# Kernel optimization log

Measured on AMD Instinct MI355X. Metric: run time of the kernel, lower is better.

Reference implementation:

```python
import jax, jax.numpy as jnp
import numpy as np

D_MODEL = 1024
NUM_HEADS = 16
HEAD_DIM = D_MODEL // NUM_HEADS


def setup_inputs() -> dict:
    key = jax.random.key(0)
    k_x, k_wqkv, k_bqkv, k_wo, k_bo = jax.random.split(key, 5)
    B, T = 2, 2048
    x = jax.random.normal(k_x, (B, T, D_MODEL), dtype=jnp.float32)
    # flax Dense default: lecun_normal kernel, zero bias; we use scaled normal for kernels
    w_qkv = jax.random.normal(k_wqkv, (D_MODEL, 3 * D_MODEL), dtype=jnp.float32) / np.sqrt(D_MODEL)
    b_qkv = jnp.zeros((3 * D_MODEL,), dtype=jnp.float32)
    w_out = jax.random.normal(k_wo, (D_MODEL, D_MODEL), dtype=jnp.float32) / np.sqrt(D_MODEL)
    b_out = jnp.zeros((D_MODEL,), dtype=jnp.float32)
    return {"x": x, "w_qkv": w_qkv, "b_qkv": b_qkv, "w_out": w_out, "b_out": b_out}


def reference(x, w_qkv, b_qkv, w_out, b_out):
    B, T, C = x.shape
    H, D = NUM_HEADS, HEAD_DIM
    qkv = x @ w_qkv + b_qkv                      # [B,T,3C]
    q, k, v = jnp.split(qkv, 3, axis=-1)         # each [B,T,C]

    def split_heads(t):
        return t.reshape(B, T, H, D).transpose(0, 2, 1, 3)  # [B,H,T,D]

    q, k, v = split_heads(q), split_heads(k), split_heads(v)
    attn = jnp.einsum('bhqd,bhkd->bhqk', q, k) / jnp.sqrt(jnp.float32(D))
    attn = jax.nn.softmax(attn, axis=-1)
    out = jnp.einsum('bhqk,bhkd->bhqd', attn, v)  # [B,H,T,D]
    out = out.transpose(0, 2, 1, 3).reshape(B, T, H * D)
    return out @ w_out + b_out
```

## Files before the change

### kernel.cpp

```cpp
#include <hip/hip_runtime.h>
#include <math.h>

#define D_MODEL 1024
#define NHEAD   16
#define HDIM    64
#define BATCH   2
#define SEQ     2048
#define M_TOTAL (BATCH*SEQ)

typedef _Float16 f16;
typedef _Float16 f16x4 __attribute__((ext_vector_type(4)));
typedef _Float16 f16x8 __attribute__((ext_vector_type(8)));
typedef float    f32x4 __attribute__((ext_vector_type(4)));

#if __has_builtin(__builtin_amdgcn_exp2f)
#define EXP2F(x) __builtin_amdgcn_exp2f(x)
#else
#define EXP2F(x) exp2f(x)
#endif

#define QSCALE 0.18033688011112042f

__device__ __forceinline__ void gl2lds16(const f16* g, f16* l) {
    __builtin_amdgcn_global_load_lds(
        (const __attribute__((address_space(1))) void*)g,
        (__attribute__((address_space(3))) void*)l,
        16, 0, 0);
}

__global__ __launch_bounds__(256) void convert_x_kernel(
    const float* __restrict__ x, f16* __restrict__ xh, int n4)
{
    int i = blockIdx.x * 256 + threadIdx.x;
    if (i >= n4) return;
    float4 v = ((const float4*)x)[i];
    f16x4 hv = {(f16)v.x, (f16)v.y, (f16)v.z, (f16)v.w};
    *(f16x4*)&xh[(size_t)i * 4] = hv;
}

__global__ __launch_bounds__(256) void convert_wt_kernel(
    const float* __restrict__ W, f16* __restrict__ Wth, int K, int N)
{
    __shared__ float tile[64][65];
    const int n0 = blockIdx.x * 64, k0 = blockIdx.y * 64;
    const int tx = threadIdx.x & 15, ty = threadIdx.x >> 4;
    #pragma unroll
    for (int i = 0; i < 4; ++i) {
        float4 v = *(const float4*)&W[(size_t)(k0 + ty + 16*i) * N + n0 + tx*4];
        tile[ty + 16*i][tx*4 + 0] = v.x;
        tile[ty + 16*i][tx*4 + 1] = v.y;
        tile[ty + 16*i][tx*4 + 2] = v.z;
        tile[ty + 16*i][tx*4 + 3] = v.w;
    }
    __syncthreads();
    #pragma unroll
    for (int i = 0; i < 4; ++i) {
        int n = ty + 16*i;
        f16x4 hv = {(f16)tile[tx*4 + 0][n], (f16)tile[tx*4 + 1][n],
                    (f16)tile[tx*4 + 2][n], (f16)tile[tx*4 + 3][n]};
        *(f16x4*)&Wth[(size_t)(n0 + n) * K + k0 + tx*4] = hv;
    }
}

__global__ __launch_bounds__(256) void gemm_qkv_mfma(
    const f16* __restrict__ Ahg, const f16* __restrict__ Bhg,
    const float* __restrict__ bias,
    f16* __restrict__ Qf, f16* __restrict__ Kf, f16* __restrict__ Vt)
{
    const int K = 1024;
    const int flat = blockIdx.x;
    const int xcd  = flat & 7;
    const int idx  = flat >> 3;
    const int m_blk = (xcd >> 1) * 8  + (idx & 7);
    const int n_blk = (xcd & 1) * 12 + (idx >> 3);
    const int n0 = n_blk * 128;
    const int m0 = m_blk * 128;
    const int tid  = threadIdx.x;
    const int lane = tid & 63;
    const int wave = tid >> 6;
    const int quad = lane >> 4;
    const int txl  = lane & 15;
    const int wm = (wave >> 1) * 64;
    const int wn = (wave & 1) * 64;

    __shared__ __align__(16) f16 sAh[128*64];
    __shared__ __align__(16) f16 sBh[128*64];

    f32x4 acc[4][4];
    #pragma unroll
    for (int i = 0; i < 4; ++i)
        #pragma unroll
        for (int j = 0; j < 4; ++j) { f32x4 z = {0.f,0.f,0.f,0.f}; acc[i][j] = z; }

    for (int kt = 0; kt < K; kt += 64) {
        __syncthreads();
        #pragma unroll
        for (int it = 0; it < 4; ++it) {
            int f = it*256 + tid;
            int r = f >> 3;
            int gc = (f & 7) ^ (r & 7);
            gl2lds16(&Ahg[(size_t)(m0 + r) * K + kt + gc*8], &sAh[f*8]);
            gl2lds16(&Bhg[(size_t)(n0 + r) * K + kt + gc*8], &sBh[f*8]);
        }
        __syncthreads();

        #pragma unroll
        for (int ks = 0; ks < 2; ++ks) {
            f16x8 ah[4], bh[4];
            #pragma unroll
            for (int i = 0; i < 4; ++i) {
                int r = wm + 16*i + txl;
                ah[i] = *(const f16x8*)&sAh[(r*8 + ((ks*4 + quad) ^ (r & 7))) * 8];
            }
            #pragma unroll
            for (int j = 0; j < 4; ++j) {
                int r = wn + 16*j + txl;
                bh[j] = *(const f16x8*)&sBh[(r*8 + ((ks*4 + quad) ^ (r & 7))) * 8];
            }
            #pragma unroll
            for (int j = 0; j < 4; ++j)
                #pragma unroll
                for (int i = 0; i < 4; ++i)
                    acc[i][j] = __builtin_amdgcn_mfma_f32_16x16x32_f16(ah[i], bh[j], acc[i][j], 0,0,0);
        }
    }

    #pragma unroll
    for (int j = 0; j < 4; ++j) {
        int n = n0 + wn + 16*j + txl;
        float bv = bias[n];
        int which = n >> 10;
        int h = (n >> 6) & 15;
        int d = n & 63;
        #pragma unroll
        for (int i = 0; i < 4; ++i) {
            int m0i = m0 + wm + 16*i + quad*4;
            int bb  = m0i >> 11;
            int t0  = m0i & (SEQ - 1);
            if (which == 2) {
                f16x4 pw = {(f16)(acc[i][j][0] + bv), (f16)(acc[i][j][1] + bv),
                            (f16)(acc[i][j][2] + bv), (f16)(acc[i][j][3] + bv)};
                *(f16x4*)&Vt[((size_t)(bb*NHEAD + h) * HDIM + d) * SEQ + t0] = pw;
            } else {
                #pragma unroll
                for (int rr = 0; rr < 4; ++rr) {
                    float v = acc[i][j][rr] + bv;
                    if (which == 0)
                        Qf[((size_t)(bb*NHEAD + h) * SEQ + t0 + rr) * HDIM + d] = (f16)(v * QSCALE);
                    else
                        Kf[((size_t)(bb*NHEAD + h) * SEQ + t0 + rr) * HDIM + d] = (f16)v;
                }
            }
        }
    }
}

__global__ __launch_bounds__(256, 4) void attn_mfma(
    const f16* __restrict__ Qf, const f16* __restrict__ Kf,
    const f16* __restrict__ Vt, f16* __restrict__ Oat)
{
    const int flat = blockIdx.x;
    const int xcd  = flat & 7;
    const int idx  = flat >> 3;
    const int bh = xcd*4 + (idx >> 5);
    const int qt = idx & 31;
    const int b  = bh >> 4;
    const int h  = bh & 15;
    const int tid  = threadIdx.x;
    const int lane = tid & 63;
    const int wave = tid >> 6;
    const int quad = lane >> 4;
    const int txl  = lane & 15;
    const int qh = wave >> 1;
    const int kh = wave & 1;

    __shared__ __align__(16) char smem[40960];
    f16* sQ  = (f16*)smem;
    f16* sKb = (f16*)(smem + 8*1024);
    f16* sVb = (f16*)(smem + 24*1024);
    float* sL      = (float*)smem;
    float* scratch = (float*)(smem + 8*1024);

    const f16* Qg = Qf + (size_t)bh * SEQ * HDIM + (size_t)qt * 64 * HDIM;
    const f16* Kg = Kf + (size_t)bh * SEQ * HDIM;
    const f16* Vg = Vt + (size_t)bh * HDIM * SEQ;

    #pragma unroll
    for (int it = 0; it < 2; ++it) {
        int f = it*256 + tid;
        int r = f >> 3;
        int gc = (f & 7) ^ (r & 7);
        gl2lds16(&Qg[(size_t)r * HDIM + gc*8], &sQ[f*8]);
        gl2lds16(&Kg[(size_t)r * HDIM + gc*8], &sKb[f*8]);
        gl2lds16(&Vg[(size_t)r * SEQ + gc*8], &sVb[f*8]);
    }
    __syncthreads();

    f16x8 bq[2][2];
    #pragma unroll
    for (int i = 0; i < 2; ++i) {
        int row = qh*32 + i*16 + txl;
        #pragma unroll
        for (int dc = 0; dc < 2; ++dc) {
            int cp = (dc*4 + quad) ^ (row & 7);
            bq[i][dc] = *(const f16x8*)&sQ[(row*8 + cp) * 8];
        }
    }
    __syncthreads();

    f32x4 oacc[2][4];
    f32x4 lmf[2];
    const f16x4 vones = {(f16)1.f, (f16)1.f, (f16)1.f, (f16)1.f};
    #pragma unroll
    for (int i = 0; i < 2; ++i) {
        f32x4 z = {0.f,0.f,0.f,0.f};
        lmf[i] = z;
        #pragma unroll
        for (int jn = 0; jn < 4; ++jn) oacc[i][jn] = z;
    }

    const int NT = SEQ / 64;
    #pragma unroll 2
    for (int t = 0; t < NT; ++t) {
        const f16* sKc = sKb + (t & 1) * 4096;
        const f16* sVc = sVb + (t & 1) * 4096;
        if (t + 1 < NT) {
            f16* sKn = sKb + ((t + 1) & 1) * 4096;
            f16* sVn = sVb + ((t + 1) & 1) * 4096;
            int kt2 = (t + 1) * 64;
            #pragma unroll
            for (int it = 0; it < 2; ++it) {
                int f = it*256 + tid;
                int r = f >> 3;
                int gc = (f & 7) ^ (r & 7);
                gl2lds16(&Kg[(size_t)(kt2 + r) * HDIM + gc*8], &sKn[f*8]);
                gl2lds16(&Vg[(size_t)r * SEQ + kt2 + gc*8], &sVn[f*8]);
            }
        }

        #pragma unroll
        for (int kg = 0; kg < 2; ++kg) {
            int krow = kh*32 + kg*16 + txl;
            f16x8 aK0 = *(const f16x8*)&sKc[(krow*8 + ((quad    ) ^ (krow & 7))) * 8];
            f16x8 aK1 = *(const f16x8*)&sKc[(krow*8 + ((quad + 4) ^ (krow & 7))) * 8];
            f16x4 bV[4];
            #pragma unroll
            for (int jn = 0; jn < 4; ++jn) {
                int d = jn*16 + txl;
                int slot = (kh*4 + kg*2 + (quad >> 1)) ^ (d & 7);
                bV[jn] = *(const f16x4*)&sVc[d*64 + slot*8 + (quad & 1)*4];
            }
            #pragma unroll
            for (int i = 0; i < 2; ++i) {
                f32x4 s = {0.f,0.f,0.f,0.f};
                s = __builtin_amdgcn_mfma_f32_16x16x32_f16(aK0, bq[i][0], s, 0,0,0);
                s = __builtin_amdgcn_mfma_f32_16x16x32_f16(aK1, bq[i][1], s, 0,0,0);
                float p0 = EXP2F(s[0]), p1 = EXP2F(s[1]);
                float p2 = EXP2F(s[2]), p3 = EXP2F(s[3]);
                f16x4 pa = {(f16)p0, (f16)p1, (f16)p2, (f16)p3};
                lmf[i] = __builtin_amdgcn_mfma_f32_16x16x16f16(pa, vones, lmf[i], 0,0,0);
                #pragma unroll
                for (int jn = 0; jn < 4; ++jn)
                    oacc[i][jn] = __builtin_amdgcn_mfma_f32_16x16x16f16(pa, bV[jn], oacc[i][jn], 0,0,0);
            }
        }
        __syncthreads();
    }

    if (txl == 0) {
        *(f32x4*)&sL[wave*32 +  0 + quad*4] = lmf[0];
        *(f32x4*)&sL[wave*32 + 16 + quad*4] = lmf[1];
    }
    __syncthreads();

    #pragma unroll
    for (int i = 0; i < 2; ++i) {
        #pragma unroll
        for (int jn = 0; jn < 4; ++jn) {
            int d = jn*16 + txl;
            *(f32x4*)&scratch[wave*1024 + d*16 + quad*4] = oacc[i][jn];
        }
        __syncthreads();
        const int d = tid & 63;
        const int g = tid >> 6;
        #pragma unroll
        for (int e = 0; e < 8; ++e) {
            int slot = g*8 + e;
            int hh = slot >> 4;
            int ql = slot & 15;
            float o = scratch[(2*hh)*1024 + d*16 + ql] + scratch[(2*hh+1)*1024 + d*16 + ql];
            float l = sL[(2*hh)*32 + i*16 + ql] + sL[(2*hh+1)*32 + i*16 + ql];
            int q = qt*64 + hh*32 + i*16 + ql;
            Oat[(size_t)(b*SEQ + q) * D_MODEL + h*HDIM + d] = (f16)(o / l);
        }
        __syncthreads();
    }
}

__global__ __launch_bounds__(256) void gemm_out_mfma(
    const f16* __restrict__ Ag, const f16* __restrict__ Bhg,
    const float* __restrict__ bias, float* __restrict__ Cg)
{
    const int K = 1024, N = 1024;
    const int flat = blockIdx.x;
    const int xcd  = flat & 7;
    const int idx  = flat >> 3;
    const int m0 = (xcd*8 + (idx & 7)) * 64;
    const int n0 = (idx >> 3) * 128;
    const int tid  = threadIdx.x;
    const int lane = tid & 63;
    const int wave = tid >> 6;
    const int quad = lane >> 4;
    const int txl  = lane & 15;
    const int wm = (wave >> 1) * 32;
    const int wn = (wave & 1) * 64;

    __shared__ __align__(16) f16 sA[64*64];
    __shared__ __align__(16) f16 sB[128*64];

    f32x4 acc[2][4];
    #pragma unroll
    for (int i = 0; i < 2; ++i)
        #pragma unroll
        for (int j = 0; j < 4; ++j) { f32x4 z = {0.f,0.f,0.f,0.f}; acc[i][j] = z; }

    for (int kt = 0; kt < K; kt += 64) {
        __syncthreads();
        #pragma unroll
        for (int it = 0; it < 2; ++it) {
            int f = it*256 + tid;
            int r = f >> 3;
            int gc = (f & 7) ^ (r & 7);
            gl2lds16(&Ag[(size_t)(m0 + r) * K + kt + gc*8], &sA[f*8]);
        }
        #pragma unroll
        for (int it = 0; it < 4; ++it) {
            int f = it*256 + tid;
            int r = f >> 3;
            int gc = (f & 7) ^ (r & 7);
            gl2lds16(&Bhg[(size_t)(n0 + r) * K + kt + gc*8], &sB[f*8]);
        }
        __syncthreads();

        #pragma unroll
        for (int ks = 0; ks < 2; ++ks) {
            f16x8 a[2], bb[4];
            #pragma unroll
            for (int i = 0; i < 2; ++i) {
                int r = wm + 16*i + txl;
                a[i] = *(const f16x8*)&sA[(r*8 + ((ks*4 + quad) ^ (r & 7))) * 8];
            }
            #pragma unroll
            for (int j = 0; j < 4; ++j) {
                int r = wn + 16*j + txl;
                bb[j] = *(const f16x8*)&sB[(r*8 + ((ks*4 + quad) ^ (r & 7))) * 8];
            }
            #pragma unroll
            for (int j = 0; j < 4; ++j)
                #pragma unroll
                for (int i = 0; i < 2; ++i)
                    acc[i][j] = __builtin_amdgcn_mfma_f32_16x16x32_f16(a[i], bb[j], acc[i][j], 0,0,0);
        }
    }

    #pragma unroll
    for (int j = 0; j < 4; ++j) {
        int n = n0 + wn + 16*j + txl;
        float bv = bias[n];
        #pragma unroll
        for (int i = 0; i < 2; ++i) {
            #pragma unroll
            for (int rr = 0; rr < 4; ++rr) {
                int m = m0 + wm + 16*i + quad*4 + rr;
                Cg[(size_t)m * N + n] = acc[i][j][rr] + bv;
            }
        }
    }
}

extern "C" void kernel_launch(void* const* d_in, const int* in_sizes, int n_in,
                              void* d_out, int out_size, void* d_ws, size_t ws_size,
                              hipStream_t stream) {
    (void)in_sizes; (void)n_in; (void)out_size; (void)ws_size;
    const float* x     = (const float*)d_in[0];
    const float* w_qkv = (const float*)d_in[1];
    const float* b_qkv = (const float*)d_in[2];
    const float* w_out = (const float*)d_in[3];
    const float* b_out = (const float*)d_in[4];
    float* out = (float*)d_out;

    const size_t MB = 1024*1024;
    char* ws = (char*)d_ws;
    f16* xh  = (f16*)(ws + 0*MB);
    f16* Wth = (f16*)(ws + 8*MB);
    f16* Woh = (f16*)(ws + 14*MB);
    f16* Qf  = (f16*)(ws + 16*MB);
    f16* Kf  = (f16*)(ws + 24*MB);
    f16* Vt  = (f16*)(ws + 32*MB);
    f16* Oat = (f16*)(ws + 40*MB);

    convert_x_kernel<<<4096, 256, 0, stream>>>(x, xh, M_TOTAL*D_MODEL/4);
    convert_wt_kernel<<<dim3(48, 16), 256, 0, stream>>>(w_qkv, Wth, 1024, 3072);
    convert_wt_kernel<<<dim3(16, 16), 256, 0, stream>>>(w_out, Woh, 1024, 1024);
    gemm_qkv_mfma<<<768, 256, 0, stream>>>(xh, Wth, b_qkv, Qf, Kf, Vt);
    attn_mfma<<<1024, 256, 0, stream>>>(Qf, Kf, Vt, Oat);
    gemm_out_mfma<<<512, 256, 0, stream>>>(Oat, Woh, b_out, out);
}
```

Before: 189.4 us.

## Vectorize epilogue stores via swapped MFMA operands and retile output GEMM

In the QKV GEMM, the Q and K blocks now swap the MFMA operands so each lane holds four consecutive columns. That lets them write f16x4 vector stores instead of scalar 2-byte stores. The attention epilogue changes to a padded row-major scratch layout with f16x8 stores of the output and a reciprocal multiply instead of a division. The output GEMM shrinks its N tile from 128 to 64, doubling the grid to 1024 blocks, and uses operand swap for float4 stores. The aim is to cut uncoalesced narrow global writes and improve occupancy, at the cost of more A reloads in the output GEMM and code duplication.

```diff
diff --git a/kernel.cpp b/kernel.cpp
--- a/kernel.cpp
+++ b/kernel.cpp
@@ -82,6 +82,7 @@
     const int txl  = lane & 15;
     const int wm = (wave >> 1) * 64;
     const int wn = (wave & 1) * 64;
+    const bool vblk = (n0 >> 10) == 2;
 
     __shared__ __align__(16) f16 sAh[128*64];
     __shared__ __align__(16) f16 sBh[128*64];
@@ -104,52 +105,86 @@
         }
         __syncthreads();
 
-        #pragma unroll
-        for (int ks = 0; ks < 2; ++ks) {
-            f16x8 ah[4], bh[4];
+        if (vblk) {
+            #pragma unroll
+            for (int ks = 0; ks < 2; ++ks) {
+                f16x8 ah[4], bh[4];
+                #pragma unroll
+                for (int i = 0; i < 4; ++i) {
+                    int r = wm + 16*i + txl;
+                    ah[i] = *(const f16x8*)&sAh[(r*8 + ((ks*4 + quad) ^ (r & 7))) * 8];
+                }
+                #pragma unroll
+                for (int j = 0; j < 4; ++j) {
+                    int r = wn + 16*j + txl;
+                    bh[j] = *(const f16x8*)&sBh[(r*8 + ((ks*4 + quad) ^ (r & 7))) * 8];
+                }
+                #pragma unroll
+                for (int j = 0; j < 4; ++j)
+                    #pragma unroll
+                    for (int i = 0; i < 4; ++i)
+                        acc[i][j] = __builtin_amdgcn_mfma_f32_16x16x32_f16(ah[i], bh[j], acc[i][j], 0,0,0);
+            }
+        } else {
+            #pragma unroll
+            for (int ks = 0; ks < 2; ++ks) {
+                f16x8 ah[4], bh[4];
+                #pragma unroll
+                for (int i = 0; i < 4; ++i) {
+                    int r = wm + 16*i + txl;
+                    ah[i] = *(const f16x8*)&sAh[(r*8 + ((ks*4 + quad) ^ (r & 7))) * 8];
+                }
+                #pragma unroll
+                for (int j = 0; j < 4; ++j) {
+                    int r = wn + 16*j + txl;
+                    bh[j] = *(const f16x8*)&sBh[(r*8 + ((ks*4 + quad) ^ (r & 7))) * 8];
+                }
+                #pragma unroll
+                for (int j = 0; j < 4; ++j)
+                    #pragma unroll
+                    for (int i = 0; i < 4; ++i)
+                        acc[i][j] = __builtin_amdgcn_mfma_f32_16x16x32_f16(bh[j], ah[i], acc[i][j], 0,0,0);
+            }
+        }
+    }
+
+    if (!vblk) {
+        const int which = n0 >> 10;
+        f16* dst = which ? Kf : Qf;
+        const float sc = which ? 1.0f : QSCALE;
+        #pragma unroll
+        for (int j = 0; j < 4; ++j) {
+            int nb = n0 + wn + 16*j + quad*4;
+            float4 bv4 = *(const float4*)&bias[nb];
+            int h2 = (nb >> 6) & 15;
+            int d  = nb & 63;
             #pragma unroll
             for (int i = 0; i < 4; ++i) {
-                int r = wm + 16*i + txl;
-                ah[i] = *(const f16x8*)&sAh[(r*8 + ((ks*4 + quad) ^ (r & 7))) * 8];
-            }
-            #pragma unroll
-            for (int j = 0; j < 4; ++j) {
-                int r = wn + 16*j + txl;
-                bh[j] = *(const f16x8*)&sBh[(r*8 + ((ks*4 + quad) ^ (r & 7))) * 8];
-            }
-            #pragma unroll
-            for (int j = 0; j < 4; ++j)
-                #pragma unroll
-                for (int i = 0; i < 4; ++i)
-                    acc[i][j] = __builtin_amdgcn_mfma_f32_16x16x32_f16(ah[i], bh[j], acc[i][j], 0,0,0);
-        }
-    }
-
-    #pragma unroll
-    for (int j = 0; j < 4; ++j) {
-        int n = n0 + wn + 16*j + txl;
-        float bv = bias[n];
-        int which = n >> 10;
-        int h = (n >> 6) & 15;
-        int d = n & 63;
-        #pragma unroll
-        for (int i = 0; i < 4; ++i) {
-            int m0i = m0 + wm + 16*i + quad*4;
-            int bb  = m0i >> 11;
-            int t0  = m0i & (SEQ - 1);
-            if (which == 2) {
+                int m  = m0 + wm + 16*i + txl;
+                int bb = m >> 11;
+                int t0 = m & (SEQ - 1);
+                f16x4 pw = {(f16)((acc[i][j][0] + bv4.x) * sc),
+                            (f16)((acc[i][j][1] + bv4.y) * sc),
+                            (f16)((acc[i][j][2] + bv4.z) * sc),
+                            (f16)((acc[i][j][3] + bv4.w) * sc)};
+                *(f16x4*)&dst[((size_t)(bb*NHEAD + h2) * SEQ + t0) * HDIM + d] = pw;
+            }
+        }
+    } else {
+        #pragma unroll
+        for (int j = 0; j < 4; ++j) {
+            int n = n0 + wn + 16*j + txl;
+            float bv = bias[n];
+            int h2 = (n >> 6) & 15;
+            int d  = n & 63;
+            #pragma unroll
+            for (int i = 0; i < 4; ++i) {
+                int m0i = m0 + wm + 16*i + quad*4;
+                int bb  = m0i >> 11;
+                int t0  = m0i & (SEQ - 1);
                 f16x4 pw = {(f16)(acc[i][j][0] + bv), (f16)(acc[i][j][1] + bv),
                             (f16)(acc[i][j][2] + bv), (f16)(acc[i][j][3] + bv)};
-                *(f16x4*)&Vt[((size_t)(bb*NHEAD + h) * HDIM + d) * SEQ + t0] = pw;
-            } else {
-                #pragma unroll
-                for (int rr = 0; rr < 4; ++rr) {
-                    float v = acc[i][j][rr] + bv;
-                    if (which == 0)
-                        Qf[((size_t)(bb*NHEAD + h) * SEQ + t0 + rr) * HDIM + d] = (f16)(v * QSCALE);
-                    else
-                        Kf[((size_t)(bb*NHEAD + h) * SEQ + t0 + rr) * HDIM + d] = (f16)v;
-                }
+                *(f16x4*)&Vt[((size_t)(bb*NHEAD + h2) * HDIM + d) * SEQ + t0] = pw;
             }
         }
     }
@@ -271,28 +306,38 @@
         *(f32x4*)&sL[wave*32 +  0 + quad*4] = lmf[0];
         *(f32x4*)&sL[wave*32 + 16 + quad*4] = lmf[1];
     }
-    __syncthreads();
+
+    const int s_  = tid >> 3;
+    const int sqh = s_ >> 4;
+    const int sql = s_ & 15;
+    const int d8  = (tid & 7) * 8;
 
     #pragma unroll
     for (int i = 0; i < 2; ++i) {
         #pragma unroll
         for (int jn = 0; jn < 4; ++jn) {
-            int d = jn*16 + txl;
-            *(f32x4*)&scratch[wave*1024 + d*16 + quad*4] = oacc[i][jn];
-        }
-        __syncthreads();
-        const int d = tid & 63;
-        const int g = tid >> 6;
-        #pragma unroll
-        for (int e = 0; e < 8; ++e) {
-            int slot = g*8 + e;
-            int hh = slot >> 4;
-            int ql = slot & 15;
-            float o = scratch[(2*hh)*1024 + d*16 + ql] + scratch[(2*hh+1)*1024 + d*16 + ql];
-            float l = sL[(2*hh)*32 + i*16 + ql] + sL[(2*hh+1)*32 + i*16 + ql];
-            int q = qt*64 + hh*32 + i*16 + ql;
-            Oat[(size_t)(b*SEQ + q) * D_MODEL + h*HDIM + d] = (f16)(o / l);
-        }
+            #pragma unroll
+            for (int rr = 0; rr < 4; ++rr)
+                scratch[wave*1088 + (quad*4 + rr)*68 + jn*16 + txl] = oacc[i][jn][rr];
+        }
+        __syncthreads();
+        float l = sL[(sqh*2)*32 + i*16 + sql] + sL[(sqh*2 + 1)*32 + i*16 + sql];
+        float rl = 1.0f / l;
+        f32x4 o0a = *(const f32x4*)&scratch[(sqh*2    )*1088 + sql*68 + d8];
+        f32x4 o0b = *(const f32x4*)&scratch[(sqh*2    )*1088 + sql*68 + d8 + 4];
+        f32x4 o1a = *(const f32x4*)&scratch[(sqh*2 + 1)*1088 + sql*68 + d8];
+        f32x4 o1b = *(const f32x4*)&scratch[(sqh*2 + 1)*1088 + sql*68 + d8 + 4];
+        f16x8 ow;
+        ow[0] = (f16)((o0a[0] + o1a[0]) * rl);
+        ow[1] = (f16)((o0a[1] + o1a[1]) * rl);
+        ow[2] = (f16)((o0a[2] + o1a[2]) * rl);
+        ow[3] = (f16)((o0a[3] + o1a[3]) * rl);
+        ow[4] = (f16)((o0b[0] + o1b[0]) * rl);
+        ow[5] = (f16)((o0b[1] + o1b[1]) * rl);
+        ow[6] = (f16)((o0b[2] + o1b[2]) * rl);
+        ow[7] = (f16)((o0b[3] + o1b[3]) * rl);
+        int q = qt*64 + sqh*32 + i*16 + sql;
+        *(f16x8*)&Oat[(size_t)(b*SEQ + q) * D_MODEL + h*HDIM + d8] = ow;
         __syncthreads();
     }
 }
@@ -306,23 +351,23 @@
     const int xcd  = flat & 7;
     const int idx  = flat >> 3;
     const int m0 = (xcd*8 + (idx & 7)) * 64;
-    const int n0 = (idx >> 3) * 128;
+    const int n0 = (idx >> 3) * 64;
     const int tid  = threadIdx.x;
     const int lane = tid & 63;
     const int wave = tid >> 6;
     const int quad = lane >> 4;
     const int txl  = lane & 15;
     const int wm = (wave >> 1) * 32;
-    const int wn = (wave & 1) * 64;
+    const int wn = (wave & 1) * 32;
 
     __shared__ __align__(16) f16 sA[64*64];
-    __shared__ __align__(16) f16 sB[128*64];
-
-    f32x4 acc[2][4];
+    __shared__ __align__(16) f16 sB[64*64];
+
+    f32x4 acc[2][2];
     #pragma unroll
     for (int i = 0; i < 2; ++i)
         #pragma unroll
-        for (int j = 0; j < 4; ++j) { f32x4 z = {0.f,0.f,0.f,0.f}; acc[i][j] = z; }
+        for (int j = 0; j < 2; ++j) { f32x4 z = {0.f,0.f,0.f,0.f}; acc[i][j] = z; }
 
     for (int kt = 0; kt < K; kt += 64) {
         __syncthreads();
@@ -332,48 +377,41 @@
             int r = f >> 3;
             int gc = (f & 7) ^ (r & 7);
             gl2lds16(&Ag[(size_t)(m0 + r) * K + kt + gc*8], &sA[f*8]);
-        }
-        #pragma unroll
-        for (int it = 0; it < 4; ++it) {
-            int f = it*256 + tid;
-            int r = f >> 3;
-            int gc = (f & 7) ^ (r & 7);
             gl2lds16(&Bhg[(size_t)(n0 + r) * K + kt + gc*8], &sB[f*8]);
         }
         __syncthreads();
 
         #pragma unroll
         for (int ks = 0; ks < 2; ++ks) {
-            f16x8 a[2], bb[4];
+            f16x8 a[2], bb[2];
             #pragma unroll
             for (int i = 0; i < 2; ++i) {
                 int r = wm + 16*i + txl;
                 a[i] = *(const f16x8*)&sA[(r*8 + ((ks*4 + quad) ^ (r & 7))) * 8];
             }
             #pragma unroll
-            for (int j = 0; j < 4; ++j) {
+            for (int j = 0; j < 2; ++j) {
                 int r = wn + 16*j + txl;
                 bb[j] = *(const f16x8*)&sB[(r*8 + ((ks*4 + quad) ^ (r & 7))) * 8];
             }
             #pragma unroll
-            for (int j = 0; j < 4; ++j)
+            for (int j = 0; j < 2; ++j)
                 #pragma unroll
                 for (int i = 0; i < 2; ++i)
-                    acc[i][j] = __builtin_amdgcn_mfma_f32_16x16x32_f16(a[i], bb[j], acc[i][j], 0,0,0);
-        }
-    }
-
-    #pragma unroll
-    for (int j = 0; j < 4; ++j) {
-        int n = n0 + wn + 16*j + txl;
-        float bv = bias[n];
+                    acc[i][j] = __builtin_amdgcn_mfma_f32_16x16x32_f16(bb[j], a[i], acc[i][j], 0,0,0);
+        }
+    }
+
+    #pragma unroll
+    for (int j = 0; j < 2; ++j) {
+        int nb = n0 + wn + 16*j + quad*4;
+        float4 bv4 = *(const float4*)&bias[nb];
         #pragma unroll
         for (int i = 0; i < 2; ++i) {
-            #pragma unroll
-            for (int rr = 0; rr < 4; ++rr) {
-                int m = m0 + wm + 16*i + quad*4 + rr;
-                Cg[(size_t)m * N + n] = acc[i][j][rr] + bv;
-            }
+            int m = m0 + wm + 16*i + txl;
+            float4 ov = {acc[i][j][0] + bv4.x, acc[i][j][1] + bv4.y,
+                         acc[i][j][2] + bv4.z, acc[i][j][3] + bv4.w};
+            *(float4*)&Cg[(size_t)m * N + nb] = ov;
         }
     }
 }
@@ -404,5 +442,5 @@
     convert_wt_kernel<<<dim3(16, 16), 256, 0, stream>>>(w_out, Woh, 1024, 1024);
     gemm_qkv_mfma<<<768, 256, 0, stream>>>(xh, Wth, b_qkv, Qf, Kf, Vt);
     attn_mfma<<<1024, 256, 0, stream>>>(Qf, Kf, Vt, Oat);
-    gemm_out_mfma<<<512, 256, 0, stream>>>(Oat, Woh, b_out, out);
-}
+    gemm_out_mfma<<<1024, 256, 0, stream>>>(Oat, Woh, b_out, out);
+}
```

Result: slower. 197.3 us (+4.2%).
